# Kernel optimization log

Measured on AMD Instinct MI355X. Metric: run time of the kernel, lower is better.

## Reference

```python
import jax, jax.numpy as jnp
import numpy as np

SEQ_LEN, BATCH, TAGS = 512, 1024, 32
START_IDX, END_IDX = 30, 31
NEG = -10000.0


def setup_inputs() -> dict:
    key = jax.random.key(0)
    k1, k2 = jax.random.split(key)
    feats = jax.random.normal(k1, (SEQ_LEN, BATCH, TAGS), dtype=jnp.float32)
    mask = jnp.ones((SEQ_LEN, BATCH), dtype=jnp.float32)
    # xavier-normal-ish transition, then apply START/END constraints as in reset_parameters
    transition = jax.random.normal(k2, (TAGS, TAGS), dtype=jnp.float32) * (2.0 / (TAGS + TAGS)) ** 0.5
    transition = transition.at[START_IDX, :].set(NEG)
    transition = transition.at[:, END_IDX].set(NEG)
    return {"feats": feats, "mask": mask, "transition": transition}


def reference(feats, mask, transition):
    # feats: (T, N, M), mask: (T, N), transition: (M, M)
    batch_size, tag_size = feats.shape[1], feats.shape[2]
    alpha0 = jnp.full((batch_size, tag_size), NEG, dtype=feats.dtype)
    alpha0 = alpha0.at[:, START_IDX].set(0.0)

    def step(alpha, inp):
        feat_t, mask_t = inp  # (N, M), (N,)
        # score[n, j, i] = alpha[n, i] + transition[j, i] + feat[n, j]
        score = alpha[:, None, :] + transition[None, :, :] + feat_t[:, :, None]
        new_alpha = jax.nn.logsumexp(score, axis=-1)  # (N, M)
        m = mask_t[:, None]
        alpha = new_alpha * m + alpha * (1.0 - m)
        return alpha, None

    alpha, _ = jax.lax.scan(step, alpha0, (feats, mask))
    alpha = alpha + transition[END_IDX][None, :]
    return jax.nn.logsumexp(alpha, axis=-1)  # (N,)
```

## Files before the change

### kernel.cpp

```cpp
#include <hip/hip_runtime.h>


constexpr int SEQ = 512, BATCH = 1024, TAGS = 32;
constexpr int CH = 8;
constexpr int NCH = (SEQ / 2) / CH;
constexpr int RINGN = 4;
constexpr int FSLOT = CH * 512;
constexpr int MSLOT = CH * 16;

#define LOG2E 1.4426950408889634f
#define LN2   0.6931471805599453f

typedef __attribute__((ext_vector_type(8))) short short8;
typedef __attribute__((ext_vector_type(4))) float float4v;
union Frag8 { unsigned u[4]; short8 v; };

__device__ __forceinline__ unsigned pk_rn(float x, float y) {
  return __builtin_amdgcn_perm(__float_as_uint(y) + 0x8000u,
                               __float_as_uint(x) + 0x8000u, 0x07060302u);
}
__device__ __forceinline__ unsigned pk_tr(float x, float y) {
  return __builtin_amdgcn_perm(__float_as_uint(y), __float_as_uint(x), 0x07060302u);
}

__device__ __forceinline__ void gld16(const float* g, float* l) {
  __builtin_amdgcn_global_load_lds((const __attribute__((address_space(1))) void*)g,
                                   (__attribute__((address_space(3))) void*)l, 16, 0, 0);
}
__device__ __forceinline__ void gld4(const float* g, float* l) {
  __builtin_amdgcn_global_load_lds((const __attribute__((address_space(1))) void*)g,
                                   (__attribute__((address_space(3))) void*)l, 4, 0, 0);
}

template <bool FWD>
__device__ __forceinline__ void produce(
    const float* __restrict__ feats, const float* __restrict__ maskp,
    float* __restrict__ FFd, float* __restrict__ MMd, int b0, int lane) {
  const int bs = lane >> 3;
  const int tg = 4 * ((lane & 7) ^ (bs & 7));
  const size_t t0 = FWD ? 0 : (size_t)(SEQ - 1);
  const float* gF0 = feats + t0 * BATCH * TAGS + (size_t)(b0 + bs) * TAGS + tg;
  const float* gF8 = gF0 + 8 * TAGS;
  const float* gM0 = maskp +
      (FWD ? (size_t)(lane >> 4) : (size_t)(SEQ - 1 - (lane >> 4))) * BATCH +
      b0 + (lane & 15);
  const ptrdiff_t fstep = FWD ? (ptrdiff_t)(BATCH * TAGS) : -(ptrdiff_t)(BATCH * TAGS);
  const ptrdiff_t mstep = FWD ? (ptrdiff_t)BATCH : -(ptrdiff_t)BATCH;

  auto FILL = [&](int k) {
    float* fb = FFd + (k & (RINGN - 1)) * FSLOT;
    float* mb = MMd + (k & (RINGN - 1)) * MSLOT;
#pragma unroll
    for (int j = 0; j < CH; ++j) {
      const ptrdiff_t o = (ptrdiff_t)(CH * k + j) * fstep;
      gld16(gF0 + o, fb + j * 512);
      gld16(gF8 + o, fb + j * 512 + 256);
    }
    gld4(gM0 + (ptrdiff_t)(CH * k) * mstep, mb);
    gld4(gM0 + (ptrdiff_t)(CH * k + 4) * mstep, mb + 64);
  };

  FILL(0); FILL(1); FILL(2);
  asm volatile("s_waitcnt vmcnt(36)" ::: "memory");
  __builtin_amdgcn_s_barrier();
  for (int k = 0; k < NCH; ++k) {
    if (k < NCH - 3) {
      FILL(k + 3);
      asm volatile("s_waitcnt vmcnt(36)" ::: "memory");
    } else if (k == NCH - 3) {
      asm volatile("s_waitcnt vmcnt(18)" ::: "memory");
    } else if (k == NCH - 2) {
      asm volatile("s_waitcnt vmcnt(0)" ::: "memory");
    }
    __builtin_amdgcn_s_barrier();
  }
  __syncthreads();
}

template <bool FWD>
__device__ __forceinline__ void consume(
    const float* __restrict__ trans, float* __restrict__ out,
    const float* __restrict__ FFd, const float* __restrict__ MMd,
    float* __restrict__ vbuf, float* __restrict__ c2buf, int b0, int lane) {
  const int s = lane & 15, q = lane >> 4;

  int sig[8];
#pragma unroll
  for (int i = 0; i < 8; ++i) sig[i] = (i < 4) ? (4 * q + i) : (16 + 4 * q + (i - 4));
  Frag8 e0, e1;
#pragma unroll
  for (int p = 0; p < 4; ++p) {
    if (FWD) {
      e0.u[p] = pk_rn(__builtin_amdgcn_exp2f(trans[s * TAGS + sig[2 * p]] * LOG2E),
                      __builtin_amdgcn_exp2f(trans[s * TAGS + sig[2 * p + 1]] * LOG2E));
      e1.u[p] = pk_rn(__builtin_amdgcn_exp2f(trans[(16 + s) * TAGS + sig[2 * p]] * LOG2E),
                      __builtin_amdgcn_exp2f(trans[(16 + s) * TAGS + sig[2 * p + 1]] * LOG2E));
    } else {
      e0.u[p] = pk_rn(__builtin_amdgcn_exp2f(trans[sig[2 * p] * TAGS + s] * LOG2E),
                      __builtin_amdgcn_exp2f(trans[sig[2 * p + 1] * TAGS + s] * LOG2E));
      e1.u[p] = pk_rn(__builtin_amdgcn_exp2f(trans[sig[2 * p] * TAGS + 16 + s] * LOG2E),
                      __builtin_amdgcn_exp2f(trans[sig[2 * p + 1] * TAGS + 16 + s] * LOG2E));
    }
  }

  float a[8];
#pragma unroll
  for (int i = 0; i < 8; ++i) {
    if (FWD) a[i] = (q == 3 && i == 6) ? 1.0f : 0.0f;
    else a[i] = __builtin_amdgcn_exp2f(
        trans[31 * TAGS + ((i < 4) ? (4 * q + i) : (16 + 4 * q + (i - 4)))] * LOG2E);
  }
  Frag8 Bf;
  Bf.u[0] = pk_tr(a[0], a[1]); Bf.u[1] = pk_tr(a[2], a[3]);
  Bf.u[2] = pk_tr(a[4], a[5]); Bf.u[3] = pk_tr(a[6], a[7]);
  float c2 = 0.f;
  const float4v zerov = {0.f, 0.f, 0.f, 0.f};

  const int off0 = s * 32 + ((q ^ (s & 7)) << 2);
  const int off1 = s * 32 + (((q + 4) ^ (s & 7)) << 2);

  float4v rA0, rA1, rB0, rB1;
  float mAv, mBv;
  float4v Fc0, Fc1;
  float mc;

  __builtin_amdgcn_s_barrier();
  __builtin_amdgcn_sched_barrier(0);
  rA0 = *(const float4v*)(FFd + 0 * 512 + off0);
  rA1 = *(const float4v*)(FFd + 0 * 512 + off1);
  mAv = MMd[0 * 16 + s];
  rB0 = *(const float4v*)(FFd + 1 * 512 + off0);
  rB1 = *(const float4v*)(FFd + 1 * 512 + off1);
  mBv = MMd[1 * 16 + s];
#pragma unroll
  for (int i = 0; i < 4; ++i) {
    Fc0[i] = __builtin_amdgcn_exp2f(rA0[i] * LOG2E);
    Fc1[i] = __builtin_amdgcn_exp2f(rA1[i] * LOG2E);
  }
  mc = mAv;

  for (int k = 0; k < NCH; ++k) {
    const float* fb = FFd + (k & (RINGN - 1)) * FSLOT;
    const float* mb = MMd + (k & (RINGN - 1)) * MSLOT;
#pragma unroll
    for (int j = 0; j < CH; ++j) {
      if (j < CH - 2) {
        float4v& c0 = (j & 1) ? rB0 : rA0;
        float4v& c1 = (j & 1) ? rB1 : rA1;
        float& cmv = (j & 1) ? mBv : mAv;
        c0 = *(const float4v*)(fb + (j + 2) * 512 + off0);
        c1 = *(const float4v*)(fb + (j + 2) * 512 + off1);
        cmv = mb[(j + 2) * 16 + s];
      }

      const bool mv = (mc != 0.0f);
      if (FWD) {
        const float4v D0 = __builtin_amdgcn_mfma_f32_16x16x32_bf16(e0.v, Bf.v, zerov, 0, 0, 0);
        const float4v D1 = __builtin_amdgcn_mfma_f32_16x16x32_bf16(e1.v, Bf.v, zerov, 0, 0, 0);
#pragma unroll
        for (int i = 0; i < 4; ++i) {
          a[i] = mv ? D0[i] * Fc0[i] : a[i];
          a[4 + i] = mv ? D1[i] * Fc1[i] : a[4 + i];
        }
      } else {
        float tb[8];
#pragma unroll
        for (int i = 0; i < 4; ++i) { tb[i] = a[i] * Fc0[i]; tb[4 + i] = a[4 + i] * Fc1[i]; }
        Frag8 Bp;
        Bp.u[0] = pk_tr(tb[0], tb[1]); Bp.u[1] = pk_tr(tb[2], tb[3]);
        Bp.u[2] = pk_tr(tb[4], tb[5]); Bp.u[3] = pk_tr(tb[6], tb[7]);
        const float4v D0 = __builtin_amdgcn_mfma_f32_16x16x32_bf16(e0.v, Bp.v, zerov, 0, 0, 0);
        const float4v D1 = __builtin_amdgcn_mfma_f32_16x16x32_bf16(e1.v, Bp.v, zerov, 0, 0, 0);
#pragma unroll
        for (int i = 0; i < 4; ++i) {
          a[i] = mv ? D0[i] : a[i];
          a[4 + i] = mv ? D1[i] : a[4 + i];
        }
      }
      if (j == CH - 1) {
        float mx = fmaxf(fmaxf(fmaxf(a[0], a[1]), fmaxf(a[2], a[3])),
                         fmaxf(fmaxf(a[4], a[5]), fmaxf(a[6], a[7])));
        mx = fmaxf(mx, __shfl_xor(mx, 16, 64));
        mx = fmaxf(mx, __shfl_xor(mx, 32, 64));
        const int ex = (int)((__float_as_uint(mx) >> 23) & 0xFFu) - 127;
        const float scl = __uint_as_float((unsigned)(127 - ex) << 23);
#pragma unroll
        for (int i = 0; i < 8; ++i) a[i] *= scl;
        c2 += (float)ex;
      }
      if (FWD) {
        Bf.u[0] = pk_tr(a[0], a[1]); Bf.u[1] = pk_tr(a[2], a[3]);
        Bf.u[2] = pk_tr(a[4], a[5]); Bf.u[3] = pk_tr(a[6], a[7]);
      }

      if (j < CH - 1) {
        const float4v& n0 = (j & 1) ? rA0 : rB0;
        const float4v& n1 = (j & 1) ? rA1 : rB1;
        const float nm = (j & 1) ? mAv : mBv;
#pragma unroll
        for (int i = 0; i < 4; ++i) {
          Fc0[i] = __builtin_amdgcn_exp2f(n0[i] * LOG2E);
          Fc1[i] = __builtin_amdgcn_exp2f(n1[i] * LOG2E);
        }
        mc = nm;
      }
    }
    asm volatile("s_waitcnt lgkmcnt(0)" ::: "memory");
    __builtin_amdgcn_s_barrier();
    __builtin_amdgcn_sched_barrier(0);
    if (k < NCH - 1) {
      const float* fn = FFd + ((k + 1) & (RINGN - 1)) * FSLOT;
      const float* mn = MMd + ((k + 1) & (RINGN - 1)) * MSLOT;
      rA0 = *(const float4v*)(fn + 0 * 512 + off0);
      rA1 = *(const float4v*)(fn + 0 * 512 + off1);
      mAv = mn[0 * 16 + s];
      rB0 = *(const float4v*)(fn + 1 * 512 + off0);
      rB1 = *(const float4v*)(fn + 1 * 512 + off1);
      mBv = mn[1 * 16 + s];
#pragma unroll
      for (int i = 0; i < 4; ++i) {
        Fc0[i] = __builtin_amdgcn_exp2f(rA0[i] * LOG2E);
        Fc1[i] = __builtin_amdgcn_exp2f(rA1[i] * LOG2E);
      }
      mc = mAv;
    }
  }

  if (!FWD) {
    float4v lo = {a[0], a[1], a[2], a[3]}, hi = {a[4], a[5], a[6], a[7]};
    *(float4v*)(vbuf + lane * 8) = lo;
    *(float4v*)(vbuf + lane * 8 + 4) = hi;
    if (lane < 16) c2buf[lane] = c2;
  }
  __syncthreads();
  if (FWD) {
    const float4v v0 = *(const float4v*)(vbuf + lane * 8);
    const float4v v1 = *(const float4v*)(vbuf + lane * 8 + 4);
    float dot = a[0] * v0[0] + a[1] * v0[1] + a[2] * v0[2] + a[3] * v0[3] +
                a[4] * v1[0] + a[5] * v1[1] + a[6] * v1[2] + a[7] * v1[3];
    dot += __shfl_xor(dot, 16, 64);
    dot += __shfl_xor(dot, 32, 64);
    if (lane < 16)
      out[b0 + lane] = LN2 * (c2 + c2buf[lane] + __builtin_amdgcn_logf(dot));
  }
}

extern "C" __global__ void __launch_bounds__(256, 1) crf_scan(
    const float* __restrict__ feats, const float* __restrict__ mask,
    const float* __restrict__ trans, float* __restrict__ out) {
  __shared__ float FF[2][RINGN][FSLOT];
  __shared__ float MM[2][RINGN][MSLOT];
  __shared__ float vbuf[512];
  __shared__ float c2buf[16];
  const int wid = threadIdx.x >> 6;
  const int lane = threadIdx.x & 63;
  const int b0 = blockIdx.x * 16;

  if (wid == 0)
    consume<true>(trans, out, &FF[0][0][0], &MM[0][0][0], vbuf, c2buf, b0, lane);
  else if (wid == 1)
    consume<false>(trans, out, &FF[1][0][0], &MM[1][0][0], vbuf, c2buf, b0, lane);
  else if (wid == 2)
    produce<true>(feats, mask, &FF[0][0][0], &MM[0][0][0], b0, lane);
  else
    produce<false>(feats, mask, &FF[1][0][0], &MM[1][0][0], b0, lane);
}

extern "C" void kernel_launch(void* const* d_in, const int* in_sizes, int n_in,
                              void* d_out, int out_size, void* d_ws, size_t ws_size,
                              hipStream_t stream) {
  const float* feats = (const float*)d_in[0];
  const float* mask  = (const float*)d_in[1];
  const float* trans = (const float*)d_in[2];
  float* out = (float*)d_out;
  hipLaunchKernelGGL(crf_scan, dim3(BATCH / 16), dim3(256), 0, stream,
                     feats, mask, trans, out);
}
```

Baseline: 120.8 us.

## Halve batch rows per block to launch twice as many workgroups

Each block now handles 8 batch rows instead of 16, so the grid doubles from 64 to 128 blocks. The LDS ring slots, global-to-LDS fills and vmcnt waits shrink to match, and consumers duplicate rows via (s & 7) so the 16-row MFMA runs half redundant. The aim is to cover more of the 256 compute units, since the serial scan is latency-bound and 64 blocks leave most CUs idle. In exchange, half of each MFMA's work is wasted and total instruction work grows.

```diff
diff --git a/kernel.cpp b/kernel.cpp
--- a/kernel.cpp
+++ b/kernel.cpp
@@ -2,11 +2,13 @@
 
 
 constexpr int SEQ = 512, BATCH = 1024, TAGS = 32;
+constexpr int BPB = 8;
 constexpr int CH = 8;
 constexpr int NCH = (SEQ / 2) / CH;
 constexpr int RINGN = 4;
-constexpr int FSLOT = CH * 512;
-constexpr int MSLOT = CH * 16;
+constexpr int SSTRIDE = BPB * TAGS;
+constexpr int FSLOT = CH * SSTRIDE;
+constexpr int MSLOT = CH * BPB;
 
 #define LOG2E 1.4426950408889634f
 #define LN2   0.6931471805599453f
@@ -40,10 +42,9 @@
   const int tg = 4 * ((lane & 7) ^ (bs & 7));
   const size_t t0 = FWD ? 0 : (size_t)(SEQ - 1);
   const float* gF0 = feats + t0 * BATCH * TAGS + (size_t)(b0 + bs) * TAGS + tg;
-  const float* gF8 = gF0 + 8 * TAGS;
   const float* gM0 = maskp +
-      (FWD ? (size_t)(lane >> 4) : (size_t)(SEQ - 1 - (lane >> 4))) * BATCH +
-      b0 + (lane & 15);
+      (FWD ? (size_t)(lane >> 3) : (size_t)(SEQ - 1 - (lane >> 3))) * BATCH +
+      b0 + (lane & 7);
   const ptrdiff_t fstep = FWD ? (ptrdiff_t)(BATCH * TAGS) : -(ptrdiff_t)(BATCH * TAGS);
   const ptrdiff_t mstep = FWD ? (ptrdiff_t)BATCH : -(ptrdiff_t)BATCH;
 
@@ -51,24 +52,20 @@
     float* fb = FFd + (k & (RINGN - 1)) * FSLOT;
     float* mb = MMd + (k & (RINGN - 1)) * MSLOT;
 #pragma unroll
-    for (int j = 0; j < CH; ++j) {
-      const ptrdiff_t o = (ptrdiff_t)(CH * k + j) * fstep;
-      gld16(gF0 + o, fb + j * 512);
-      gld16(gF8 + o, fb + j * 512 + 256);
-    }
+    for (int j = 0; j < CH; ++j)
+      gld16(gF0 + (ptrdiff_t)(CH * k + j) * fstep, fb + j * SSTRIDE);
     gld4(gM0 + (ptrdiff_t)(CH * k) * mstep, mb);
-    gld4(gM0 + (ptrdiff_t)(CH * k + 4) * mstep, mb + 64);
   };
 
   FILL(0); FILL(1); FILL(2);
-  asm volatile("s_waitcnt vmcnt(36)" ::: "memory");
+  asm volatile("s_waitcnt vmcnt(18)" ::: "memory");
   __builtin_amdgcn_s_barrier();
   for (int k = 0; k < NCH; ++k) {
     if (k < NCH - 3) {
       FILL(k + 3);
-      asm volatile("s_waitcnt vmcnt(36)" ::: "memory");
+      asm volatile("s_waitcnt vmcnt(18)" ::: "memory");
     } else if (k == NCH - 3) {
-      asm volatile("s_waitcnt vmcnt(18)" ::: "memory");
+      asm volatile("s_waitcnt vmcnt(9)" ::: "memory");
     } else if (k == NCH - 2) {
       asm volatile("s_waitcnt vmcnt(0)" ::: "memory");
     }
@@ -126,12 +123,12 @@
 
   __builtin_amdgcn_s_barrier();
   __builtin_amdgcn_sched_barrier(0);
-  rA0 = *(const float4v*)(FFd + 0 * 512 + off0);
-  rA1 = *(const float4v*)(FFd + 0 * 512 + off1);
-  mAv = MMd[0 * 16 + s];
-  rB0 = *(const float4v*)(FFd + 1 * 512 + off0);
-  rB1 = *(const float4v*)(FFd + 1 * 512 + off1);
-  mBv = MMd[1 * 16 + s];
+  rA0 = *(const float4v*)(FFd + 0 * SSTRIDE + off0);
+  rA1 = *(const float4v*)(FFd + 0 * SSTRIDE + off1);
+  mAv = MMd[0 * BPB + (s & 7)];
+  rB0 = *(const float4v*)(FFd + 1 * SSTRIDE + off0);
+  rB1 = *(const float4v*)(FFd + 1 * SSTRIDE + off1);
+  mBv = MMd[1 * BPB + (s & 7)];
 #pragma unroll
   for (int i = 0; i < 4; ++i) {
     Fc0[i] = __builtin_amdgcn_exp2f(rA0[i] * LOG2E);
@@ -148,9 +145,9 @@
         float4v& c0 = (j & 1) ? rB0 : rA0;
         float4v& c1 = (j & 1) ? rB1 : rA1;
         float& cmv = (j & 1) ? mBv : mAv;
-        c0 = *(const float4v*)(fb + (j + 2) * 512 + off0);
-        c1 = *(const float4v*)(fb + (j + 2) * 512 + off1);
-        cmv = mb[(j + 2) * 16 + s];
+        c0 = *(const float4v*)(fb + (j + 2) * SSTRIDE + off0);
+        c1 = *(const float4v*)(fb + (j + 2) * SSTRIDE + off1);
+        cmv = mb[(j + 2) * BPB + (s & 7)];
       }
 
       const bool mv = (mc != 0.0f);
@@ -211,12 +208,12 @@
     if (k < NCH - 1) {
       const float* fn = FFd + ((k + 1) & (RINGN - 1)) * FSLOT;
       const float* mn = MMd + ((k + 1) & (RINGN - 1)) * MSLOT;
-      rA0 = *(const float4v*)(fn + 0 * 512 + off0);
-      rA1 = *(const float4v*)(fn + 0 * 512 + off1);
-      mAv = mn[0 * 16 + s];
-      rB0 = *(const float4v*)(fn + 1 * 512 + off0);
-      rB1 = *(const float4v*)(fn + 1 * 512 + off1);
-      mBv = mn[1 * 16 + s];
+      rA0 = *(const float4v*)(fn + 0 * SSTRIDE + off0);
+      rA1 = *(const float4v*)(fn + 0 * SSTRIDE + off1);
+      mAv = mn[0 * BPB + (s & 7)];
+      rB0 = *(const float4v*)(fn + 1 * SSTRIDE + off0);
+      rB1 = *(const float4v*)(fn + 1 * SSTRIDE + off1);
+      mBv = mn[1 * BPB + (s & 7)];
 #pragma unroll
       for (int i = 0; i < 4; ++i) {
         Fc0[i] = __builtin_amdgcn_exp2f(rA0[i] * LOG2E);
@@ -230,7 +227,7 @@
     float4v lo = {a[0], a[1], a[2], a[3]}, hi = {a[4], a[5], a[6], a[7]};
     *(float4v*)(vbuf + lane * 8) = lo;
     *(float4v*)(vbuf + lane * 8 + 4) = hi;
-    if (lane < 16) c2buf[lane] = c2;
+    if (lane < 8) c2buf[lane] = c2;
   }
   __syncthreads();
   if (FWD) {
@@ -240,7 +237,7 @@
                 a[4] * v1[0] + a[5] * v1[1] + a[6] * v1[2] + a[7] * v1[3];
     dot += __shfl_xor(dot, 16, 64);
     dot += __shfl_xor(dot, 32, 64);
-    if (lane < 16)
+    if (lane < 8)
       out[b0 + lane] = LN2 * (c2 + c2buf[lane] + __builtin_amdgcn_logf(dot));
   }
 }
@@ -254,7 +251,7 @@
   __shared__ float c2buf[16];
   const int wid = threadIdx.x >> 6;
   const int lane = threadIdx.x & 63;
-  const int b0 = blockIdx.x * 16;
+  const int b0 = blockIdx.x * BPB;
 
   if (wid == 0)
     consume<true>(trans, out, &FF[0][0][0], &MM[0][0][0], vbuf, c2buf, b0, lane);
@@ -273,6 +270,6 @@
   const float* mask  = (const float*)d_in[1];
   const float* trans = (const float*)d_in[2];
   float* out = (float*)d_out;
-  hipLaunchKernelGGL(crf_scan, dim3(BATCH / 16), dim3(256), 0, stream,
+  hipLaunchKernelGGL(crf_scan, dim3(BATCH / BPB), dim3(256), 0, stream,
                      feats, mask, trans, out);
 }
```

Result: no change. 119.8 us (-0.8%).
